# Kernel optimization log

Hardware: AMD Instinct MI355X
Metric: run time of the kernel (lower is better)

Reference implementation:

```python
import jax, jax.numpy as jnp
import numpy as np

N_NODES = 50000
N_EDGES = 600000
D_IN = 128
D_HID = 1024
D_OUT = 128


def setup_inputs() -> dict:
    key = jax.random.key(0)
    ks = jax.random.split(key, 8)
    feat = jax.random.normal(ks[0], (N_NODES, D_IN), dtype=jnp.float32)
    edge_feat = jax.random.normal(ks[1], (N_EDGES, D_IN), dtype=jnp.float32)
    src = jax.random.randint(ks[2], (N_EDGES,), 0, N_NODES, dtype=jnp.int32)
    dst = jax.random.randint(ks[3], (N_EDGES,), 0, N_NODES, dtype=jnp.int32)
    W1 = jax.random.normal(ks[4], (D_IN, D_HID), dtype=jnp.float32) * (1.0 / np.sqrt(D_IN))
    b1 = jnp.zeros((D_HID,), dtype=jnp.float32)
    W2 = jax.random.normal(ks[5], (D_HID, D_OUT), dtype=jnp.float32) * (1.0 / np.sqrt(D_HID))
    b2 = jnp.zeros((D_OUT,), dtype=jnp.float32)
    return {"feat": feat, "edge_feat": edge_feat, "src": src, "dst": dst,
            "W1": W1, "b1": b1, "W2": W2, "b2": b2}


def reference(feat, edge_feat, src, dst, W1, b1, W2, b2):
    # DGL u_add_e: message m_e = h_src(e) + e_feat(e)   [E, D_IN]
    messages = feat[src] + edge_feat
    # reduce sum over incoming edges at each destination node -> [N, D_IN]
    h = jax.ops.segment_sum(messages, dst, num_segments=N_NODES)
    # 2-layer MLP
    h = jax.nn.relu(h @ W1 + b1)
    return h @ W2 + b2
```

## Files before the change

### kernel.cpp

```cpp
#include <hip/hip_runtime.h>
#include <hip/hip_bf16.h>

#define N_NODES 50000
#define N_EDGES 600000
#define D_IN    128
#define D_HID   1024
#define D_OUT   128

#define WS_PAIRS  0
#define WS_OFF    4800000
#define WS_CURSOR 5000016
#define WS_DEG    5200016
#define WS_BSUM   5400016
#define WS_W1T    5401040
#define WS_W2T    5663184

typedef short bf16x8 __attribute__((ext_vector_type(8)));
typedef float f32x4  __attribute__((ext_vector_type(4)));
typedef int   i32x2  __attribute__((ext_vector_type(2)));

__global__ __launch_bounds__(256) void hist_kernel(
    const int* __restrict__ dst, int* __restrict__ deg)
{
    int e = blockIdx.x * blockDim.x + threadIdx.x;
    if (e < N_EDGES) atomicAdd(&deg[dst[e]], 1);
}

__global__ __launch_bounds__(256) void scan1_kernel(
    const int* __restrict__ deg, int* __restrict__ bsum)
{
    __shared__ int red[256];
    int t = threadIdx.x;
    int idx = blockIdx.x * 256 + t;
    red[t] = (idx < N_NODES) ? deg[idx] : 0;
    __syncthreads();
    for (int s = 128; s > 0; s >>= 1) {
        if (t < s) red[t] += red[t + s];
        __syncthreads();
    }
    if (t == 0) bsum[blockIdx.x] = red[0];
}

#define SCAN_NB 196
__global__ __launch_bounds__(256) void scan2_kernel(
    int* __restrict__ bsum, int* __restrict__ off)
{
    __shared__ int sh[256];
    int t = threadIdx.x;
    int v = (t < SCAN_NB) ? bsum[t] : 0;
    sh[t] = v;
    __syncthreads();
    for (int ofs = 1; ofs < 256; ofs <<= 1) {
        int u = (t >= ofs) ? sh[t - ofs] : 0;
        __syncthreads();
        sh[t] += u;
        __syncthreads();
    }
    if (t < SCAN_NB) bsum[t] = sh[t] - v;
    if (t == 255) off[N_NODES] = sh[255];
}

__global__ __launch_bounds__(256) void scan3_kernel(
    const int* __restrict__ deg, const int* __restrict__ bsum,
    int* __restrict__ off, int* __restrict__ cursor)
{
    __shared__ int sh[256];
    int t = threadIdx.x;
    int idx = blockIdx.x * 256 + t;
    int v = (idx < N_NODES) ? deg[idx] : 0;
    sh[t] = v;
    __syncthreads();
    for (int ofs = 1; ofs < 256; ofs <<= 1) {
        int u = (t >= ofs) ? sh[t - ofs] : 0;
        __syncthreads();
        sh[t] += u;
        __syncthreads();
    }
    if (idx < N_NODES) {
        int ex = bsum[blockIdx.x] + sh[t] - v;
        off[idx] = ex;
        cursor[idx] = ex;
    }
}

__global__ __launch_bounds__(256) void fill_kernel(
    const int* __restrict__ dst, const int* __restrict__ src,
    int* __restrict__ cursor, int* __restrict__ pairs)
{
    int e = blockIdx.x * blockDim.x + threadIdx.x;
    if (e < N_EDGES) {
        int s = src[e];
        int pos = atomicAdd(&cursor[dst[e]], 1);
        i32x2 v; v.x = e; v.y = s;
        *(i32x2*)(pairs + 2 * (size_t)pos) = v;
    }
}

__global__ __launch_bounds__(256) void transpose_cvt2_kernel(
    const float* __restrict__ W1, __hip_bfloat16* __restrict__ w1t,
    const float* __restrict__ W2, __hip_bfloat16* __restrict__ w2t)
{
    __shared__ float tile[32][33];
    int b = blockIdx.x;
    const float* in;
    __hip_bfloat16* outp;
    int rows, cols, c0, r0;
    if (b < 128) {
        in = W1; outp = w1t; rows = D_IN; cols = D_HID;
        c0 = (b & 31) * 32; r0 = (b >> 5) * 32;
    } else {
        int bb = b - 128;
        in = W2; outp = w2t; rows = D_HID; cols = D_OUT;
        c0 = (bb & 3) * 32; r0 = (bb >> 2) * 32;
    }
    int tx = threadIdx.x & 31, ty = threadIdx.x >> 5;
    #pragma unroll
    for (int i = 0; i < 32; i += 8)
        tile[ty + i][tx] = in[(size_t)(r0 + ty + i) * cols + (c0 + tx)];
    __syncthreads();
    #pragma unroll
    for (int i = 0; i < 32; i += 8)
        outp[(size_t)(c0 + ty + i) * rows + (r0 + tx)] =
            __float2bfloat16(tile[tx][ty + i]);
}

#define HS_STRIDE 136
#define QS_STRIDE 72

__global__ __launch_bounds__(256) void fused_gnn_kernel(
    const float* __restrict__ feat,
    const float* __restrict__ edge_feat,
    const int*   __restrict__ pairs,
    const int*   __restrict__ off,
    const __hip_bfloat16* __restrict__ w1t,
    const float* __restrict__ b1,
    const __hip_bfloat16* __restrict__ w2t,
    const float* __restrict__ b2,
    float* __restrict__ out)
{
    __shared__ __align__(16) short h_s[64 * HS_STRIDE];
    __shared__ __align__(16) short q_s[2][64 * QS_STRIDE];
    __shared__ int off_s[65];

    const int t    = threadIdx.x;
    const int wv   = t >> 6;
    const int lane = t & 63;
    const int half = lane >> 4;
    const int lid  = lane & 15;
    const int nb   = blockIdx.x * 64;

    const short* w1s = (const short*)w1t;
    const short* w2s = (const short*)w2t;

    if (t < 65) {
        int oidx = nb + t;
        off_s[t] = off[oidx > N_NODES ? N_NODES : oidx];
    }
    __syncthreads();

    {
        const int r0  = wv * 16;
        int cur = r0;
        int nxt = off_s[r0 + 1];
        const int i0  = off_s[r0];
        const int end = off_s[r0 + 16];
        float2 acc = make_float2(0.f, 0.f);

        #define FLUSH_ROW() do {                                            \
            __hip_bfloat162 hv_;                                            \
            hv_.x = __float2bfloat16(acc.x);                                \
            hv_.y = __float2bfloat16(acc.y);                                \
            *(__hip_bfloat162*)&h_s[cur * HS_STRIDE + lane * 2] = hv_;      \
            acc.x = 0.f; acc.y = 0.f;                                       \
            ++cur; nxt = off_s[cur + 1];                                    \
        } while (0)

        #define EDGE_ACC(K, EV, GV) do {                                    \
            while (i + (K) >= nxt) FLUSH_ROW();                             \
            acc.x += EV.x + GV.x;                                           \
            acc.y += EV.y + GV.y;                                           \
        } while (0)

        int i = i0;
        for (; i + 8 <= end; i += 8) {
            i32x2 p0 = *(const i32x2*)(pairs + 2 * (size_t)(i + 0));
            i32x2 p1 = *(const i32x2*)(pairs + 2 * (size_t)(i + 1));
            i32x2 p2 = *(const i32x2*)(pairs + 2 * (size_t)(i + 2));
            i32x2 p3 = *(const i32x2*)(pairs + 2 * (size_t)(i + 3));
            i32x2 p4 = *(const i32x2*)(pairs + 2 * (size_t)(i + 4));
            i32x2 p5 = *(const i32x2*)(pairs + 2 * (size_t)(i + 5));
            i32x2 p6 = *(const i32x2*)(pairs + 2 * (size_t)(i + 6));
            i32x2 p7 = *(const i32x2*)(pairs + 2 * (size_t)(i + 7));
            float2 e0 = ((const float2*)(edge_feat + (size_t)p0.x * D_IN))[lane];
            float2 g0 = ((const float2*)(feat      + (size_t)p0.y * D_IN))[lane];
            float2 e1 = ((const float2*)(edge_feat + (size_t)p1.x * D_IN))[lane];
            float2 g1 = ((const float2*)(feat      + (size_t)p1.y * D_IN))[lane];
            float2 e2 = ((const float2*)(edge_feat + (size_t)p2.x * D_IN))[lane];
            float2 g2 = ((const float2*)(feat      + (size_t)p2.y * D_IN))[lane];
            float2 e3 = ((const float2*)(edge_feat + (size_t)p3.x * D_IN))[lane];
            float2 g3 = ((const float2*)(feat      + (size_t)p3.y * D_IN))[lane];
            float2 e4 = ((const float2*)(edge_feat + (size_t)p4.x * D_IN))[lane];
            float2 g4 = ((const float2*)(feat      + (size_t)p4.y * D_IN))[lane];
            float2 e5 = ((const float2*)(edge_feat + (size_t)p5.x * D_IN))[lane];
            float2 g5 = ((const float2*)(feat      + (size_t)p5.y * D_IN))[lane];
            float2 e6 = ((const float2*)(edge_feat + (size_t)p6.x * D_IN))[lane];
            float2 g6 = ((const float2*)(feat      + (size_t)p6.y * D_IN))[lane];
            float2 e7 = ((const float2*)(edge_feat + (size_t)p7.x * D_IN))[lane];
            float2 g7 = ((const float2*)(feat      + (size_t)p7.y * D_IN))[lane];
            EDGE_ACC(0, e0, g0);
            EDGE_ACC(1, e1, g1);
            EDGE_ACC(2, e2, g2);
            EDGE_ACC(3, e3, g3);
            EDGE_ACC(4, e4, g4);
            EDGE_ACC(5, e5, g5);
            EDGE_ACC(6, e6, g6);
            EDGE_ACC(7, e7, g7);
        }
        for (; i < end; ++i) {
            i32x2 p = *(const i32x2*)(pairs + 2 * (size_t)i);
            float2 e = ((const float2*)(edge_feat + (size_t)p.x * D_IN))[lane];
            float2 g = ((const float2*)(feat      + (size_t)p.y * D_IN))[lane];
            EDGE_ACC(0, e, g);
        }
        while (cur < r0 + 16) {
            __hip_bfloat162 hv_;
            hv_.x = __float2bfloat16(acc.x);
            hv_.y = __float2bfloat16(acc.y);
            *(__hip_bfloat162*)&h_s[cur * HS_STRIDE + lane * 2] = hv_;
            acc.x = 0.f; acc.y = 0.f;
            ++cur;
        }
        #undef EDGE_ACC
        #undef FLUSH_ROW
    }
    __syncthreads();

    bf16x8 afrag[4][4];
    #pragma unroll
    for (int mt = 0; mt < 4; ++mt)
        #pragma unroll
        for (int ks = 0; ks < 4; ++ks)
            afrag[mt][ks] = *(const bf16x8*)&h_s[(mt * 16 + lid) * HS_STRIDE + ks * 32 + half * 8];

    f32x4 acc[4][2];
    #pragma unroll
    for (int mt = 0; mt < 4; ++mt) {
        acc[mt][0] = f32x4{0.f, 0.f, 0.f, 0.f};
        acc[mt][1] = f32x4{0.f, 0.f, 0.f, 0.f};
    }

    const int ncol1 = wv * 16 + lid;

    int pb = 0;
    for (int jb = 0; jb < D_HID; jb += 64, pb ^= 1) {
        float bias = b1[jb + ncol1];
        bf16x8 bfrag[4];
        #pragma unroll
        for (int ks = 0; ks < 4; ++ks)
            bfrag[ks] = *(const bf16x8*)&w1s[(size_t)(jb + ncol1) * 128 + ks * 32 + half * 8];

        f32x4 c1[4];
        #pragma unroll
        for (int mt = 0; mt < 4; ++mt) {
            f32x4 c = f32x4{bias, bias, bias, bias};
            #pragma unroll
            for (int ks = 0; ks < 4; ++ks)
                c = __builtin_amdgcn_mfma_f32_16x16x32_bf16(afrag[mt][ks], bfrag[ks], c, 0, 0, 0);
            c1[mt] = c;
        }

        #pragma unroll
        for (int mt = 0; mt < 4; ++mt) {
            #pragma unroll
            for (int r = 0; r < 4; ++r) {
                float v = fmaxf(c1[mt][r], 0.f);
                __hip_bfloat16 bv = __float2bfloat16(v);
                q_s[pb][(mt * 16 + half * 4 + r) * QS_STRIDE + wv * 16 + lid] = *(short*)&bv;
            }
        }
        __syncthreads();

        bf16x8 a2f[4][2];
        #pragma unroll
        for (int mt = 0; mt < 4; ++mt)
            #pragma unroll
            for (int ks = 0; ks < 2; ++ks)
                a2f[mt][ks] = *(const bf16x8*)&q_s[pb][(mt * 16 + lid) * QS_STRIDE + ks * 32 + half * 8];

        #pragma unroll
        for (int nt = 0; nt < 2; ++nt) {
            #pragma unroll
            for (int ks = 0; ks < 2; ++ks) {
                bf16x8 b2f = *(const bf16x8*)&w2s[(size_t)(wv * 32 + nt * 16 + lid) * 1024 + jb + ks * 32 + half * 8];
                #pragma unroll
                for (int mt = 0; mt < 4; ++mt)
                    acc[mt][nt] = __builtin_amdgcn_mfma_f32_16x16x32_bf16(a2f[mt][ks], b2f, acc[mt][nt], 0, 0, 0);
            }
        }
    }

    #pragma unroll
    for (int nt = 0; nt < 2; ++nt) {
        int col = wv * 32 + nt * 16 + lid;
        float bv = b2[col];
        #pragma unroll
        for (int mt = 0; mt < 4; ++mt) {
            #pragma unroll
            for (int r = 0; r < 4; ++r) {
                int row = nb + mt * 16 + half * 4 + r;
                if (row < N_NODES)
                    out[(size_t)row * D_OUT + col] = acc[mt][nt][r] + bv;
            }
        }
    }
}

extern "C" void kernel_launch(void* const* d_in, const int* in_sizes, int n_in,
                              void* d_out, int out_size, void* d_ws, size_t ws_size,
                              hipStream_t stream) {
    const float* feat      = (const float*)d_in[0];
    const float* edge_feat = (const float*)d_in[1];
    const int*   src       = (const int*)d_in[2];
    const int*   dst       = (const int*)d_in[3];
    const float* W1        = (const float*)d_in[4];
    const float* b1        = (const float*)d_in[5];
    const float* W2        = (const float*)d_in[6];
    const float* b2        = (const float*)d_in[7];
    float* out = (float*)d_out;

    char* ws = (char*)d_ws;
    int*   pairs  = (int*)(ws + WS_PAIRS);
    int*   off    = (int*)(ws + WS_OFF);
    int*   cursor = (int*)(ws + WS_CURSOR);
    int*   deg    = (int*)(ws + WS_DEG);
    int*   bsum   = (int*)(ws + WS_BSUM);
    __hip_bfloat16* w1t = (__hip_bfloat16*)(ws + WS_W1T);
    __hip_bfloat16* w2t = (__hip_bfloat16*)(ws + WS_W2T);

    hipMemsetAsync(deg, 0, (size_t)N_NODES * sizeof(int), stream);

    hist_kernel<<<(N_EDGES + 255) / 256, 256, 0, stream>>>(dst, deg);
    scan1_kernel<<<SCAN_NB, 256, 0, stream>>>(deg, bsum);
    scan2_kernel<<<1, 256, 0, stream>>>(bsum, off);
    scan3_kernel<<<SCAN_NB, 256, 0, stream>>>(deg, bsum, off, cursor);
    fill_kernel<<<(N_EDGES + 255) / 256, 256, 0, stream>>>(dst, src, cursor, pairs);

    transpose_cvt2_kernel<<<256, 256, 0, stream>>>(W1, w1t, W2, w2t);

    fused_gnn_kernel<<<(N_NODES + 63) / 64, 256, 0, stream>>>(
        feat, edge_feat, pairs, off, w1t, b1, w2t, b2, out);
}
```

Baseline: 637.8 us.

## Split fused gather+MLP into separate per-node gather and MFMA MLP kernels

The fused kernel, where each wave walked edges for 16 destination rows with per-edge row-boundary checks, is split in two. A gather kernel assigns one wave per node, uses four independent accumulators for more memory-level parallelism, and writes a bf16 h buffer to workspace. The MLP kernel then loads h tiles from global memory. This gives finer load balancing and removes branchy flush logic, at the cost of an extra kernel launch and a 12.8MB intermediate round-trip.

```diff
diff --git a/kernel.cpp b/kernel.cpp
--- a/kernel.cpp
+++ b/kernel.cpp
@@ -7,13 +7,14 @@
 #define D_HID   1024
 #define D_OUT   128
 
-#define WS_PAIRS  0
-#define WS_OFF    4800000
-#define WS_CURSOR 5000016
-#define WS_DEG    5200016
-#define WS_BSUM   5400016
-#define WS_W1T    5401040
-#define WS_W2T    5663184
+#define WS_H      0
+#define WS_PAIRS  12800000
+#define WS_OFF    17600000
+#define WS_CURSOR 17800016
+#define WS_DEG    18000016
+#define WS_BSUM   18200016
+#define WS_W1T    18201040
+#define WS_W2T    18463184
 
 typedef short bf16x8 __attribute__((ext_vector_type(8)));
 typedef float f32x4  __attribute__((ext_vector_type(4)));
@@ -124,14 +125,86 @@
             __float2bfloat16(tile[tx][ty + i]);
 }
 
-#define HS_STRIDE 136
-#define QS_STRIDE 72
-
-__global__ __launch_bounds__(256) void fused_gnn_kernel(
+__global__ __launch_bounds__(256) void gather_kernel(
     const float* __restrict__ feat,
     const float* __restrict__ edge_feat,
     const int*   __restrict__ pairs,
     const int*   __restrict__ off,
+    __hip_bfloat16* __restrict__ hbf)
+{
+    const int wv   = threadIdx.x >> 6;
+    const int lane = threadIdx.x & 63;
+    const int n = blockIdx.x * 4 + wv;
+    if (n >= N_NODES) return;
+
+    int i   = __builtin_amdgcn_readfirstlane(off[n]);
+    int end = __builtin_amdgcn_readfirstlane(off[n + 1]);
+
+    float2 a0 = make_float2(0.f, 0.f), a1 = a0, a2 = a0, a3 = a0;
+
+    for (; i + 8 <= end; i += 8) {
+        i32x2 p0 = *(const i32x2*)(pairs + 2 * (size_t)(i + 0));
+        i32x2 p1 = *(const i32x2*)(pairs + 2 * (size_t)(i + 1));
+        i32x2 p2 = *(const i32x2*)(pairs + 2 * (size_t)(i + 2));
+        i32x2 p3 = *(const i32x2*)(pairs + 2 * (size_t)(i + 3));
+        i32x2 p4 = *(const i32x2*)(pairs + 2 * (size_t)(i + 4));
+        i32x2 p5 = *(const i32x2*)(pairs + 2 * (size_t)(i + 5));
+        i32x2 p6 = *(const i32x2*)(pairs + 2 * (size_t)(i + 6));
+        i32x2 p7 = *(const i32x2*)(pairs + 2 * (size_t)(i + 7));
+        float2 e0 = ((const float2*)(edge_feat + (size_t)p0.x * D_IN))[lane];
+        float2 g0 = ((const float2*)(feat      + (size_t)p0.y * D_IN))[lane];
+        float2 e1 = ((const float2*)(edge_feat + (size_t)p1.x * D_IN))[lane];
+        float2 g1 = ((const float2*)(feat      + (size_t)p1.y * D_IN))[lane];
+        float2 e2 = ((const float2*)(edge_feat + (size_t)p2.x * D_IN))[lane];
+        float2 g2 = ((const float2*)(feat      + (size_t)p2.y * D_IN))[lane];
+        float2 e3 = ((const float2*)(edge_feat + (size_t)p3.x * D_IN))[lane];
+        float2 g3 = ((const float2*)(feat      + (size_t)p3.y * D_IN))[lane];
+        float2 e4 = ((const float2*)(edge_feat + (size_t)p4.x * D_IN))[lane];
+        float2 g4 = ((const float2*)(feat      + (size_t)p4.y * D_IN))[lane];
+        float2 e5 = ((const float2*)(edge_feat + (size_t)p5.x * D_IN))[lane];
+        float2 g5 = ((const float2*)(feat      + (size_t)p5.y * D_IN))[lane];
+        float2 e6 = ((const float2*)(edge_feat + (size_t)p6.x * D_IN))[lane];
+        float2 g6 = ((const float2*)(feat      + (size_t)p6.y * D_IN))[lane];
+        float2 e7 = ((const float2*)(edge_feat + (size_t)p7.x * D_IN))[lane];
+        float2 g7 = ((const float2*)(feat      + (size_t)p7.y * D_IN))[lane];
+        a0.x += e0.x + g0.x;  a0.y += e0.y + g0.y;
+        a1.x += e1.x + g1.x;  a1.y += e1.y + g1.y;
+        a2.x += e2.x + g2.x;  a2.y += e2.y + g2.y;
+        a3.x += e3.x + g3.x;  a3.y += e3.y + g3.y;
+        a0.x += e4.x + g4.x;  a0.y += e4.y + g4.y;
+        a1.x += e5.x + g5.x;  a1.y += e5.y + g5.y;
+        a2.x += e6.x + g6.x;  a2.y += e6.y + g6.y;
+        a3.x += e7.x + g7.x;  a3.y += e7.y + g7.y;
+    }
+    for (; i + 2 <= end; i += 2) {
+        i32x2 p0 = *(const i32x2*)(pairs + 2 * (size_t)(i + 0));
+        i32x2 p1 = *(const i32x2*)(pairs + 2 * (size_t)(i + 1));
+        float2 e0 = ((const float2*)(edge_feat + (size_t)p0.x * D_IN))[lane];
+        float2 g0 = ((const float2*)(feat      + (size_t)p0.y * D_IN))[lane];
+        float2 e1 = ((const float2*)(edge_feat + (size_t)p1.x * D_IN))[lane];
+        float2 g1 = ((const float2*)(feat      + (size_t)p1.y * D_IN))[lane];
+        a0.x += e0.x + g0.x;  a0.y += e0.y + g0.y;
+        a1.x += e1.x + g1.x;  a1.y += e1.y + g1.y;
+    }
+    if (i < end) {
+        i32x2 p = *(const i32x2*)(pairs + 2 * (size_t)i);
+        float2 e = ((const float2*)(edge_feat + (size_t)p.x * D_IN))[lane];
+        float2 g = ((const float2*)(feat      + (size_t)p.y * D_IN))[lane];
+        a0.x += e.x + g.x;  a0.y += e.y + g.y;
+    }
+    float sx = (a0.x + a1.x) + (a2.x + a3.x);
+    float sy = (a0.y + a1.y) + (a2.y + a3.y);
+    __hip_bfloat162 hv;
+    hv.x = __float2bfloat16(sx);
+    hv.y = __float2bfloat16(sy);
+    ((__hip_bfloat162*)(hbf + (size_t)n * D_IN))[lane] = hv;
+}
+
+#define HS_STRIDE 136
+#define QS_STRIDE 72
+
+__global__ __launch_bounds__(256) void mlp_mfma_kernel(
+    const __hip_bfloat16* __restrict__ hbf,
     const __hip_bfloat16* __restrict__ w1t,
     const float* __restrict__ b1,
     const __hip_bfloat16* __restrict__ w2t,
@@ -140,7 +213,6 @@
 {
     __shared__ __align__(16) short h_s[64 * HS_STRIDE];
     __shared__ __align__(16) short q_s[2][64 * QS_STRIDE];
-    __shared__ int off_s[65];
 
     const int t    = threadIdx.x;
     const int wv   = t >> 6;
@@ -149,89 +221,16 @@
     const int lid  = lane & 15;
     const int nb   = blockIdx.x * 64;
 
+    const short* hs  = (const short*)hbf;
     const short* w1s = (const short*)w1t;
     const short* w2s = (const short*)w2t;
 
-    if (t < 65) {
-        int oidx = nb + t;
-        off_s[t] = off[oidx > N_NODES ? N_NODES : oidx];
-    }
-    __syncthreads();
-
-    {
-        const int r0  = wv * 16;
-        int cur = r0;
-        int nxt = off_s[r0 + 1];
-        const int i0  = off_s[r0];
-        const int end = off_s[r0 + 16];
-        float2 acc = make_float2(0.f, 0.f);
-
-        #define FLUSH_ROW() do {                                            \
-            __hip_bfloat162 hv_;                                            \
-            hv_.x = __float2bfloat16(acc.x);                                \
-            hv_.y = __float2bfloat16(acc.y);                                \
-            *(__hip_bfloat162*)&h_s[cur * HS_STRIDE + lane * 2] = hv_;      \
-            acc.x = 0.f; acc.y = 0.f;                                       \
-            ++cur; nxt = off_s[cur + 1];                                    \
-        } while (0)
-
-        #define EDGE_ACC(K, EV, GV) do {                                    \
-            while (i + (K) >= nxt) FLUSH_ROW();                             \
-            acc.x += EV.x + GV.x;                                           \
-            acc.y += EV.y + GV.y;                                           \
-        } while (0)
-
-        int i = i0;
-        for (; i + 8 <= end; i += 8) {
-            i32x2 p0 = *(const i32x2*)(pairs + 2 * (size_t)(i + 0));
-            i32x2 p1 = *(const i32x2*)(pairs + 2 * (size_t)(i + 1));
-            i32x2 p2 = *(const i32x2*)(pairs + 2 * (size_t)(i + 2));
-            i32x2 p3 = *(const i32x2*)(pairs + 2 * (size_t)(i + 3));
-            i32x2 p4 = *(const i32x2*)(pairs + 2 * (size_t)(i + 4));
-            i32x2 p5 = *(const i32x2*)(pairs + 2 * (size_t)(i + 5));
-            i32x2 p6 = *(const i32x2*)(pairs + 2 * (size_t)(i + 6));
-            i32x2 p7 = *(const i32x2*)(pairs + 2 * (size_t)(i + 7));
-            float2 e0 = ((const float2*)(edge_feat + (size_t)p0.x * D_IN))[lane];
-            float2 g0 = ((const float2*)(feat      + (size_t)p0.y * D_IN))[lane];
-            float2 e1 = ((const float2*)(edge_feat + (size_t)p1.x * D_IN))[lane];
-            float2 g1 = ((const float2*)(feat      + (size_t)p1.y * D_IN))[lane];
-            float2 e2 = ((const float2*)(edge_feat + (size_t)p2.x * D_IN))[lane];
-            float2 g2 = ((const float2*)(feat      + (size_t)p2.y * D_IN))[lane];
-            float2 e3 = ((const float2*)(edge_feat + (size_t)p3.x * D_IN))[lane];
-            float2 g3 = ((const float2*)(feat      + (size_t)p3.y * D_IN))[lane];
-            float2 e4 = ((const float2*)(edge_feat + (size_t)p4.x * D_IN))[lane];
-            float2 g4 = ((const float2*)(feat      + (size_t)p4.y * D_IN))[lane];
-            float2 e5 = ((const float2*)(edge_feat + (size_t)p5.x * D_IN))[lane];
-            float2 g5 = ((const float2*)(feat      + (size_t)p5.y * D_IN))[lane];
-            float2 e6 = ((const float2*)(edge_feat + (size_t)p6.x * D_IN))[lane];
-            float2 g6 = ((const float2*)(feat      + (size_t)p6.y * D_IN))[lane];
-            float2 e7 = ((const float2*)(edge_feat + (size_t)p7.x * D_IN))[lane];
-            float2 g7 = ((const float2*)(feat      + (size_t)p7.y * D_IN))[lane];
-            EDGE_ACC(0, e0, g0);
-            EDGE_ACC(1, e1, g1);
-            EDGE_ACC(2, e2, g2);
-            EDGE_ACC(3, e3, g3);
-            EDGE_ACC(4, e4, g4);
-            EDGE_ACC(5, e5, g5);
-            EDGE_ACC(6, e6, g6);
-            EDGE_ACC(7, e7, g7);
-        }
-        for (; i < end; ++i) {
-            i32x2 p = *(const i32x2*)(pairs + 2 * (size_t)i);
-            float2 e = ((const float2*)(edge_feat + (size_t)p.x * D_IN))[lane];
-            float2 g = ((const float2*)(feat      + (size_t)p.y * D_IN))[lane];
-            EDGE_ACC(0, e, g);
-        }
-        while (cur < r0 + 16) {
-            __hip_bfloat162 hv_;
-            hv_.x = __float2bfloat16(acc.x);
-            hv_.y = __float2bfloat16(acc.y);
-            *(__hip_bfloat162*)&h_s[cur * HS_STRIDE + lane * 2] = hv_;
-            acc.x = 0.f; acc.y = 0.f;
-            ++cur;
-        }
-        #undef EDGE_ACC
-        #undef FLUSH_ROW
+    for (int u = t; u < 64 * 16; u += 256) {
+        int r = u >> 4, c = u & 15;
+        int row = nb + r;
+        uint4 v = make_uint4(0u, 0u, 0u, 0u);
+        if (row < N_NODES) v = ((const uint4*)(hs + (size_t)row * 128))[c];
+        *(uint4*)&h_s[r * HS_STRIDE + c * 8] = v;
     }
     __syncthreads();
 
@@ -329,6 +328,7 @@
     float* out = (float*)d_out;
 
     char* ws = (char*)d_ws;
+    __hip_bfloat16* hbf = (__hip_bfloat16*)(ws + WS_H);
     int*   pairs  = (int*)(ws + WS_PAIRS);
     int*   off    = (int*)(ws + WS_OFF);
     int*   cursor = (int*)(ws + WS_CURSOR);
@@ -347,6 +347,9 @@
 
     transpose_cvt2_kernel<<<256, 256, 0, stream>>>(W1, w1t, W2, w2t);
 
-    fused_gnn_kernel<<<(N_NODES + 63) / 64, 256, 0, stream>>>(
-        feat, edge_feat, pairs, off, w1t, b1, w2t, b2, out);
-}
+    gather_kernel<<<(N_NODES + 3) / 4, 256, 0, stream>>>(
+        feat, edge_feat, pairs, off, hbf);
+
+    mlp_mfma_kernel<<<(N_NODES + 63) / 64, 256, 0, stream>>>(
+        hbf, w1t, b1, w2t, b2, out);
+}
```

Measured after the change: 611.6 us. 4.1% less time.
